# Kernel optimization log

Measured on AMD Instinct MI355X. Metric: run time of the kernel, lower is better.

Reference implementation:

```python
import jax, jax.numpy as jnp
import numpy as np

NEG_INF = -1e9
LEAKY_SLOPE = 0.2


def setup_inputs() -> dict:
    key = jax.random.key(0)
    k1, k2, k3, k4, k5 = jax.random.split(key, 5)
    B, N, F_in, F_out = 8, 2048, 256, 256
    x = jax.random.normal(k1, (B, N, F_in), dtype=jnp.float32)
    adj = jax.random.randint(k2, (B, N, N), 0, 2, dtype=jnp.int32)
    W = jax.random.normal(k3, (F_out, F_in), dtype=jnp.float32) * 0.05
    a_src = jax.random.normal(k4, (F_out,), dtype=jnp.float32) * 0.05
    a_dst = jax.random.normal(k5, (F_out,), dtype=jnp.float32) * 0.05
    return {"x": x, "adj": adj, "W": W, "a_src": a_src, "a_dst": a_dst}


def reference(x, adj, W, a_src, a_dst):
    # h: (B, N, F_out)
    h = jnp.einsum("bnf,of->bno", x, W)
    # a([h_i ; h_j]) == h_i @ a_src + h_j @ a_dst  (avoids O(N^2, 2F) concat)
    s_src = h @ a_src  # (B, N) score contribution of row node i
    s_dst = h @ a_dst  # (B, N) score contribution of col node j
    e = s_src[:, :, None] + s_dst[:, None, :]  # (B, N, N)
    e = jax.nn.leaky_relu(e, negative_slope=LEAKY_SLOPE)
    e = jnp.where(adj == 0, jnp.float32(NEG_INF), e)
    alpha = jax.nn.softmax(e, axis=-1)  # dropout is identity in eval mode
    h_prime = jnp.einsum("bij,bjo->bio", alpha, h)
    return h_prime
```

## Files before the change

### kernel.cpp

```cpp
#include <hip/hip_runtime.h>
#include <hip/hip_bf16.h>
#include <cstdint>
#include <cstddef>

typedef __attribute__((ext_vector_type(8))) short short8;
typedef __attribute__((ext_vector_type(4))) short short4v;
typedef __attribute__((ext_vector_type(4))) float floatx4;

#define LOG2E 1.44269504088896340736f

__device__ __forceinline__ unsigned short f2bf(float f) {
    unsigned u = __float_as_uint(f);
    u += 0x7FFFu + ((u >> 16) & 1u);
    return (unsigned short)(u >> 16);
}
__device__ __forceinline__ float bf2f(unsigned short s) {
    return __uint_as_float(((unsigned)s) << 16);
}

__global__ __launch_bounds__(256) void wprep(const float* __restrict__ W,
                                             unsigned short* __restrict__ Wb) {
    int t = blockIdx.x * 256 + threadIdx.x;
    float4 v = ((const float4*)W)[t];
    short4v s;
    s[0] = (short)f2bf(v.x); s[1] = (short)f2bf(v.y);
    s[2] = (short)f2bf(v.z); s[3] = (short)f2bf(v.w);
    ((short4v*)Wb)[t] = s;
}

__global__ __launch_bounds__(256) void gemm_h(const float* __restrict__ x,
                                              const unsigned short* __restrict__ Wb,
                                              unsigned short* __restrict__ hT) {
    const int w = threadIdx.x >> 6, lane = threadIdx.x & 63;
    const int q = lane >> 4, t16 = lane & 15;
    const int jrow = blockIdx.x * 64 + w * 16 + t16;
    const int ob   = blockIdx.y * 64;

    floatx4 acc[4] = {};
#pragma unroll
    for (int kb = 0; kb < 8; ++kb) {
        const int k0 = kb * 32 + q * 8;
        const float4* ax = (const float4*)(x + (size_t)jrow * 256 + k0);
        float4 a0 = ax[0], a1 = ax[1];
        short8 af;
        af[0] = (short)f2bf(a0.x); af[1] = (short)f2bf(a0.y);
        af[2] = (short)f2bf(a0.z); af[3] = (short)f2bf(a0.w);
        af[4] = (short)f2bf(a1.x); af[5] = (short)f2bf(a1.y);
        af[6] = (short)f2bf(a1.z); af[7] = (short)f2bf(a1.w);
#pragma unroll
        for (int ct = 0; ct < 4; ++ct) {
            short8 bf = *(const short8*)(Wb + (size_t)(ob + ct * 16 + t16) * 256 + k0);
            acc[ct] = __builtin_amdgcn_mfma_f32_16x16x32_bf16(af, bf, acc[ct], 0, 0, 0);
        }
    }
    const int jbase = blockIdx.x * 64 + w * 16 + q * 4;
    const int b = jbase >> 11, jj = jbase & 2047;
#pragma unroll
    for (int ct = 0; ct < 4; ++ct) {
        const int o = ob + ct * 16 + t16;
        short4v sv;
        sv[0] = (short)f2bf(acc[ct][0]);
        sv[1] = (short)f2bf(acc[ct][1]);
        sv[2] = (short)f2bf(acc[ct][2]);
        sv[3] = (short)f2bf(acc[ct][3]);
        *(short4v*)(hT + ((size_t)b * 256 + o) * 2048 + jj) = sv;
    }
}

__global__ __launch_bounds__(512) void s_kernel(const unsigned short* __restrict__ hT,
                                                const float* __restrict__ a_src,
                                                const float* __restrict__ a_dst,
                                                float* __restrict__ s_src,
                                                float* __restrict__ s_dst) {
    const int jl = threadIdx.x & 63;
    const int og = threadIdx.x >> 6;
    const int jg = blockIdx.x * 64 + jl;
    const int b = jg >> 11, jj = jg & 2047;
    const unsigned short* base = hT + (size_t)b * 256 * 2048 + jj;
    float ps = 0.f, pd = 0.f;
#pragma unroll 8
    for (int u = 0; u < 32; ++u) {
        const int o = og * 32 + u;
        float h = bf2f(base[(size_t)o * 2048]);
        ps = __fmaf_rn(h, a_src[o], ps);
        pd = __fmaf_rn(h, a_dst[o], pd);
    }
    __shared__ float rs[512], rd[512];
    rs[threadIdx.x] = ps; rd[threadIdx.x] = pd;
    __syncthreads();
    if (threadIdx.x < 64) {
        float a = 0.f, d = 0.f;
#pragma unroll
        for (int g = 0; g < 8; ++g) { a += rs[g * 64 + jl]; d += rd[g * 64 + jl]; }
        s_src[jg] = a; s_dst[jg] = d;
    }
}

__global__ __launch_bounds__(256, 2) void attn(const unsigned short* __restrict__ hT,
                                               const int* __restrict__ adj,
                                               const float* __restrict__ s_src,
                                               const float* __restrict__ s_dst,
                                               float* __restrict__ out) {
    const int tid = threadIdx.x;
    const int w = tid >> 6, lane = tid & 63;
    const int q = lane >> 4, t16 = lane & 15;
    const int b = blockIdx.y;
    const int i0 = blockIdx.x * 32;

    __shared__ float sd_lds[2048];
    __shared__ float si_lds[32];
    __shared__ unsigned short p_lds[2][32][136];
    __shared__ float lred[32][33];
    __shared__ float rl_lds[32];

    const float* sdb = s_dst + (size_t)b * 2048;
#pragma unroll
    for (int k = 0; k < 2; ++k) {
        int idx = (k * 256 + tid) * 4;
        float4 v = *(const float4*)(sdb + idx);
        v.x *= LOG2E; v.y *= LOG2E; v.z *= LOG2E; v.w *= LOG2E;
        *(float4*)(&sd_lds[idx]) = v;
    }
    if (tid < 32) si_lds[tid] = s_src[(size_t)b * 2048 + i0 + tid] * LOG2E;
    __syncthreads();

    const int rg = tid >> 5;
    const int jc = (tid & 31) * 4;
    const int* adjb = adj + ((size_t)b * 2048 + i0) * 2048;
    float si[4];
#pragma unroll
    for (int k = 0; k < 4; ++k) si[k] = si_lds[rg + 8 * k];

    float lsum[4] = {0.f, 0.f, 0.f, 0.f};
    int4 adjv[4];

    const unsigned short* hTw = hT + ((size_t)b * 256 + w * 64 + t16) * 2048 + q * 8;
    floatx4 accO[2][4] = {};

#pragma unroll
    for (int k = 0; k < 4; ++k)
        adjv[k] = *(const int4*)(adjb + (size_t)(rg + 8 * k) * 2048 + jc);
    {
        float4 sdv = *(const float4*)(&sd_lds[jc]);
        float sdl[4] = {sdv.x, sdv.y, sdv.z, sdv.w};
        unsigned short* pb = &p_lds[0][0][0];
#pragma unroll
        for (int k = 0; k < 4; ++k) {
            int mv[4] = {adjv[k].x, adjv[k].y, adjv[k].z, adjv[k].w};
            short4v sv;
#pragma unroll
            for (int e = 0; e < 4; ++e) {
                float t = si[k] + sdl[e];
                float lr = fmaxf(t, 0.2f * t);
                float pe = __builtin_amdgcn_exp2f(lr);
                pe = (mv[e] != 0) ? pe : 0.0f;
                unsigned short pu = f2bf(pe);
                sv[e] = (short)pu;
                lsum[k] += bf2f(pu);
            }
            *(short4v*)(pb + (rg + 8 * k) * 136 + jc) = sv;
        }
    }
    __syncthreads();

    for (int c = 0; c < 16; ++c) {
        if (c < 15) {
#pragma unroll
            for (int k = 0; k < 4; ++k)
                adjv[k] = *(const int4*)(adjb + (size_t)(rg + 8 * k) * 2048 + (c + 1) * 128 + jc);
        }
        const unsigned short* pb = &p_lds[c & 1][0][0];
#pragma unroll
        for (int ks = 0; ks < 4; ++ks) {
            short8 bf0 = *(const short8*)(pb + t16 * 136 + ks * 32 + q * 8);
            short8 bf1 = *(const short8*)(pb + (16 + t16) * 136 + ks * 32 + q * 8);
#pragma unroll
            for (int ct = 0; ct < 4; ++ct) {
                short8 af = *(const short8*)(hTw + (size_t)ct * 16 * 2048 + c * 128 + ks * 32);
                accO[0][ct] = __builtin_amdgcn_mfma_f32_16x16x32_bf16(af, bf0, accO[0][ct], 0, 0, 0);
                accO[1][ct] = __builtin_amdgcn_mfma_f32_16x16x32_bf16(af, bf1, accO[1][ct], 0, 0, 0);
            }
        }
        if (c < 15) {
            float4 sdv = *(const float4*)(&sd_lds[(c + 1) * 128 + jc]);
            float sdl[4] = {sdv.x, sdv.y, sdv.z, sdv.w};
            unsigned short* pw = &p_lds[(c + 1) & 1][0][0];
#pragma unroll
            for (int k = 0; k < 4; ++k) {
                int mv[4] = {adjv[k].x, adjv[k].y, adjv[k].z, adjv[k].w};
                short4v sv;
#pragma unroll
                for (int e = 0; e < 4; ++e) {
                    float t = si[k] + sdl[e];
                    float lr = fmaxf(t, 0.2f * t);
                    float pe = __builtin_amdgcn_exp2f(lr);
                    pe = (mv[e] != 0) ? pe : 0.0f;
                    unsigned short pu = f2bf(pe);
                    sv[e] = (short)pu;
                    lsum[k] += bf2f(pu);
                }
                *(short4v*)(pw + (rg + 8 * k) * 136 + jc) = sv;
            }
        }
        __syncthreads();
    }

#pragma unroll
    for (int k = 0; k < 4; ++k) lred[rg + 8 * k][tid & 31] = lsum[k];
    __syncthreads();
    if (tid < 32) {
        float s = 0.f;
#pragma unroll
        for (int u = 0; u < 32; ++u) s += lred[tid][u];
        rl_lds[tid] = (s > 0.f) ? 1.0f / s : 0.0f;
    }
    __syncthreads();

#pragma unroll
    for (int it = 0; it < 2; ++it) {
        const float rl = rl_lds[it * 16 + t16];
        float* orow = out + ((size_t)b * 2048 + i0 + it * 16 + t16) * 256 + w * 64 + q * 4;
#pragma unroll
        for (int ct = 0; ct < 4; ++ct) {
            floatx4 v = accO[it][ct] * rl;
            *(floatx4*)(orow + ct * 16) = v;
        }
    }
}

extern "C" void kernel_launch(void* const* d_in, const int* in_sizes, int n_in,
                              void* d_out, int out_size, void* d_ws, size_t ws_size,
                              hipStream_t stream) {
    const float* x     = (const float*)d_in[0];
    const int*   adj   = (const int*)d_in[1];
    const float* W     = (const float*)d_in[2];
    const float* a_src = (const float*)d_in[3];
    const float* a_dst = (const float*)d_in[4];
    float* out = (float*)d_out;

    unsigned short* hT = (unsigned short*)d_ws;
    float* s_src = (float*)((char*)d_ws + (size_t)8 * 1024 * 1024);
    float* s_dst = s_src + 16384;
    unsigned short* Wb = (unsigned short*)(s_dst + 16384);

    wprep<<<64, 256, 0, stream>>>(W, Wb);
    gemm_h<<<dim3(256, 4), 256, 0, stream>>>(x, Wb, hT);
    s_kernel<<<256, 512, 0, stream>>>(hT, a_src, a_dst, s_src, s_dst);
    attn<<<dim3(64, 8), 256, 0, stream>>>(hT, adj, s_src, s_dst, out);
}
```

Baseline: 291.2 us.

## Fuse score projection into GEMM and retile attention with LDS-staged h and 64-row tiles

The projection GEMM now computes all 256 output features per block, staging bf16 W through LDS. It computes s_src/s_dst in its epilogue with shuffle reductions, which removes the separate s_kernel launch and its strided re-read of hT. The attention kernel switches to 64 query rows per block with 32-column chunks, staging h tiles in double-buffered LDS instead of reading them straight from global memory. The intent is to cut redundant global traffic and a launch. The cost is larger per-block register and LDS use, plus a barrier on every one of 64 chunks instead of 16.

```diff
diff --git a/kernel.cpp b/kernel.cpp
--- a/kernel.cpp
+++ b/kernel.cpp
@@ -6,6 +6,7 @@
 typedef __attribute__((ext_vector_type(8))) short short8;
 typedef __attribute__((ext_vector_type(4))) short short4v;
 typedef __attribute__((ext_vector_type(4))) float floatx4;
+typedef unsigned short ushort_t;
 
 #define LOG2E 1.44269504088896340736f
 
@@ -19,7 +20,7 @@
 }
 
 __global__ __launch_bounds__(256) void wprep(const float* __restrict__ W,
-                                             unsigned short* __restrict__ Wb) {
+                                             ushort_t* __restrict__ Wb) {
     int t = blockIdx.x * 256 + threadIdx.x;
     float4 v = ((const float4*)W)[t];
     short4v s;
@@ -29,35 +30,60 @@
 }
 
 __global__ __launch_bounds__(256) void gemm_h(const float* __restrict__ x,
-                                              const unsigned short* __restrict__ Wb,
-                                              unsigned short* __restrict__ hT) {
-    const int w = threadIdx.x >> 6, lane = threadIdx.x & 63;
+                                              const ushort_t* __restrict__ Wb,
+                                              ushort_t* __restrict__ hT,
+                                              const float* __restrict__ a_src,
+                                              const float* __restrict__ a_dst,
+                                              float* __restrict__ s_src,
+                                              float* __restrict__ s_dst) {
+    const int tid = threadIdx.x;
+    const int w = tid >> 6, lane = tid & 63;
     const int q = lane >> 4, t16 = lane & 15;
+
+    __shared__ ushort_t wt[256][72];
+
     const int jrow = blockIdx.x * 64 + w * 16 + t16;
-    const int ob   = blockIdx.y * 64;
-
-    floatx4 acc[4] = {};
+    const float* xr = x + (size_t)jrow * 256 + q * 8;
+    short8 af[8];
 #pragma unroll
     for (int kb = 0; kb < 8; ++kb) {
-        const int k0 = kb * 32 + q * 8;
-        const float4* ax = (const float4*)(x + (size_t)jrow * 256 + k0);
-        float4 a0 = ax[0], a1 = ax[1];
-        short8 af;
-        af[0] = (short)f2bf(a0.x); af[1] = (short)f2bf(a0.y);
-        af[2] = (short)f2bf(a0.z); af[3] = (short)f2bf(a0.w);
-        af[4] = (short)f2bf(a1.x); af[5] = (short)f2bf(a1.y);
-        af[6] = (short)f2bf(a1.z); af[7] = (short)f2bf(a1.w);
-#pragma unroll
-        for (int ct = 0; ct < 4; ++ct) {
-            short8 bf = *(const short8*)(Wb + (size_t)(ob + ct * 16 + t16) * 256 + k0);
-            acc[ct] = __builtin_amdgcn_mfma_f32_16x16x32_bf16(af, bf, acc[ct], 0, 0, 0);
-        }
-    }
+        float4 v0 = *(const float4*)(xr + kb * 32);
+        float4 v1 = *(const float4*)(xr + kb * 32 + 4);
+        short8 a;
+        a[0] = (short)f2bf(v0.x); a[1] = (short)f2bf(v0.y);
+        a[2] = (short)f2bf(v0.z); a[3] = (short)f2bf(v0.w);
+        a[4] = (short)f2bf(v1.x); a[5] = (short)f2bf(v1.y);
+        a[6] = (short)f2bf(v1.z); a[7] = (short)f2bf(v1.w);
+        af[kb] = a;
+    }
+
+    floatx4 acc[16] = {};
+#pragma unroll
+    for (int kp = 0; kp < 4; ++kp) {
+        if (kp) __syncthreads();
+#pragma unroll
+        for (int r = 0; r < 8; ++r) {
+            int G = tid + 256 * r;
+            int row = G >> 3, g = G & 7;
+            int4 wv = *(const int4*)(Wb + (size_t)row * 256 + kp * 64 + g * 8);
+            *(int4*)(&wt[row][g * 8]) = wv;
+        }
+        __syncthreads();
+#pragma unroll
+        for (int ks = 0; ks < 2; ++ks) {
+#pragma unroll
+            for (int ct = 0; ct < 16; ++ct) {
+                short8 bf = *(const short8*)(&wt[ct * 16 + t16][ks * 32 + q * 8]);
+                acc[ct] = __builtin_amdgcn_mfma_f32_16x16x32_bf16(af[kp * 2 + ks], bf, acc[ct], 0, 0, 0);
+            }
+        }
+    }
+
     const int jbase = blockIdx.x * 64 + w * 16 + q * 4;
     const int b = jbase >> 11, jj = jbase & 2047;
 #pragma unroll
-    for (int ct = 0; ct < 4; ++ct) {
-        const int o = ob + ct * 16 + t16;
+    for (int ct = 0; ct < 16; ++ct) {
+        const int o = ct * 16 + t16;
         short4v sv;
         sv[0] = (short)f2bf(acc[ct][0]);
         sv[1] = (short)f2bf(acc[ct][1]);
@@ -65,53 +91,51 @@
         sv[3] = (short)f2bf(acc[ct][3]);
         *(short4v*)(hT + ((size_t)b * 256 + o) * 2048 + jj) = sv;
     }
-}
-
-__global__ __launch_bounds__(512) void s_kernel(const unsigned short* __restrict__ hT,
-                                                const float* __restrict__ a_src,
-                                                const float* __restrict__ a_dst,
-                                                float* __restrict__ s_src,
-                                                float* __restrict__ s_dst) {
-    const int jl = threadIdx.x & 63;
-    const int og = threadIdx.x >> 6;
-    const int jg = blockIdx.x * 64 + jl;
-    const int b = jg >> 11, jj = jg & 2047;
-    const unsigned short* base = hT + (size_t)b * 256 * 2048 + jj;
-    float ps = 0.f, pd = 0.f;
-#pragma unroll 8
-    for (int u = 0; u < 32; ++u) {
-        const int o = og * 32 + u;
-        float h = bf2f(base[(size_t)o * 2048]);
-        ps = __fmaf_rn(h, a_src[o], ps);
-        pd = __fmaf_rn(h, a_dst[o], pd);
-    }
-    __shared__ float rs[512], rd[512];
-    rs[threadIdx.x] = ps; rd[threadIdx.x] = pd;
-    __syncthreads();
-    if (threadIdx.x < 64) {
-        float a = 0.f, d = 0.f;
-#pragma unroll
-        for (int g = 0; g < 8; ++g) { a += rs[g * 64 + jl]; d += rd[g * 64 + jl]; }
-        s_src[jg] = a; s_dst[jg] = d;
-    }
-}
-
-__global__ __launch_bounds__(256, 2) void attn(const unsigned short* __restrict__ hT,
-                                               const int* __restrict__ adj,
-                                               const float* __restrict__ s_src,
-                                               const float* __restrict__ s_dst,
-                                               float* __restrict__ out) {
+
+    float psv[4] = {}, pdv[4] = {};
+#pragma unroll
+    for (int ct = 0; ct < 16; ++ct) {
+        const int o = ct * 16 + t16;
+        float as = a_src[o], ad = a_dst[o];
+#pragma unroll
+        for (int r = 0; r < 4; ++r) {
+            psv[r] = __fmaf_rn(acc[ct][r], as, psv[r]);
+            pdv[r] = __fmaf_rn(acc[ct][r], ad, pdv[r]);
+        }
+    }
+#pragma unroll
+    for (int m = 1; m < 16; m <<= 1) {
+#pragma unroll
+        for (int r = 0; r < 4; ++r) {
+            psv[r] += __shfl_xor(psv[r], m);
+            pdv[r] += __shfl_xor(pdv[r], m);
+        }
+    }
+    if (t16 == 0) {
+#pragma unroll
+        for (int r = 0; r < 4; ++r) {
+            s_src[jbase + r] = psv[r];
+            s_dst[jbase + r] = pdv[r];
+        }
+    }
+}
+
+__global__ __launch_bounds__(256) void attn(const ushort_t* __restrict__ hT,
+                                            const int* __restrict__ adj,
+                                            const float* __restrict__ s_src,
+                                            const float* __restrict__ s_dst,
+                                            float* __restrict__ out) {
     const int tid = threadIdx.x;
     const int w = tid >> 6, lane = tid & 63;
     const int q = lane >> 4, t16 = lane & 15;
-    const int b = blockIdx.y;
-    const int i0 = blockIdx.x * 32;
-
-    __shared__ float sd_lds[2048];
-    __shared__ float si_lds[32];
-    __shared__ unsigned short p_lds[2][32][136];
-    __shared__ float lred[32][33];
-    __shared__ float rl_lds[32];
+    const int b = blockIdx.x;
+    const int i0 = blockIdx.y * 64;
+
+    __shared__ ushort_t hts[2][256][40];
+    __shared__ ushort_t ps[2][64][40];
+    __shared__ float sdl[2048];
+    __shared__ float lred[64][5];
+    __shared__ float rll[64];
 
     const float* sdb = s_dst + (size_t)b * 2048;
 #pragma unroll
@@ -119,110 +143,85 @@
         int idx = (k * 256 + tid) * 4;
         float4 v = *(const float4*)(sdb + idx);
         v.x *= LOG2E; v.y *= LOG2E; v.z *= LOG2E; v.w *= LOG2E;
-        *(float4*)(&sd_lds[idx]) = v;
-    }
-    if (tid < 32) si_lds[tid] = s_src[(size_t)b * 2048 + i0 + tid] * LOG2E;
+        *(float4*)(&sdl[idx]) = v;
+    }
+
+    const int prow = tid & 63, jh = tid >> 6;
+    const float si = s_src[(size_t)b * 2048 + i0 + prow] * LOG2E;
+    const int* adjr = adj + ((size_t)b * 2048 + i0 + prow) * 2048 + jh * 8;
+    const ushort_t* hTg = hT + ((size_t)b * 256 + tid) * 2048;
+
+    const int osub = (w & 1) * 128, ih = (w >> 1) * 32;
+
+    floatx4 acc[8][2] = {};
+    float lsum = 0.f;
+    int4 hreg[4];
+    int4 a0, a1;
+
+#pragma unroll
+    for (int g = 0; g < 4; ++g)
+        hreg[g] = *(const int4*)(hTg + g * 8);
+    a0 = *(const int4*)(adjr);
+    a1 = *(const int4*)(adjr + 4);
     __syncthreads();
 
-    const int rg = tid >> 5;
-    const int jc = (tid & 31) * 4;
-    const int* adjb = adj + ((size_t)b * 2048 + i0) * 2048;
-    float si[4];
-#pragma unroll
-    for (int k = 0; k < 4; ++k) si[k] = si_lds[rg + 8 * k];
-
-    float lsum[4] = {0.f, 0.f, 0.f, 0.f};
-    int4 adjv[4];
-
-    const unsigned short* hTw = hT + ((size_t)b * 256 + w * 64 + t16) * 2048 + q * 8;
-    floatx4 accO[2][4] = {};
-
-#pragma unroll
-    for (int k = 0; k < 4; ++k)
-        adjv[k] = *(const int4*)(adjb + (size_t)(rg + 8 * k) * 2048 + jc);
-    {
-        float4 sdv = *(const float4*)(&sd_lds[jc]);
-        float sdl[4] = {sdv.x, sdv.y, sdv.z, sdv.w};
-        unsigned short* pb = &p_lds[0][0][0];
-#pragma unroll
-        for (int k = 0; k < 4; ++k) {
-            int mv[4] = {adjv[k].x, adjv[k].y, adjv[k].z, adjv[k].w};
-            short4v sv;
-#pragma unroll
-            for (int e = 0; e < 4; ++e) {
-                float t = si[k] + sdl[e];
+    for (int c = 0; c < 64; ++c) {
+        const int buf = c & 1;
+#pragma unroll
+        for (int g = 0; g < 4; ++g)
+            *(int4*)(&hts[buf][tid][g * 8]) = hreg[g];
+        {
+            float4 s0 = *(const float4*)(&sdl[c * 32 + jh * 8]);
+            float4 s1 = *(const float4*)(&sdl[c * 32 + jh * 8 + 4]);
+            float sdv[8] = {s0.x, s0.y, s0.z, s0.w, s1.x, s1.y, s1.z, s1.w};
+            int mv[8] = {a0.x, a0.y, a0.z, a0.w, a1.x, a1.y, a1.z, a1.w};
+            short8 pv;
+#pragma unroll
+            for (int e = 0; e < 8; ++e) {
+                float t = si + sdv[e];
                 float lr = fmaxf(t, 0.2f * t);
                 float pe = __builtin_amdgcn_exp2f(lr);
                 pe = (mv[e] != 0) ? pe : 0.0f;
-                unsigned short pu = f2bf(pe);
-                sv[e] = (short)pu;
-                lsum[k] += bf2f(pu);
+                unsigned short u = f2bf(pe);
+                lsum += bf2f(u);
+                pv[e] = (short)u;
             }
-            *(short4v*)(pb + (rg + 8 * k) * 136 + jc) = sv;
-        }
-    }
+            *(short8*)(&ps[buf][prow][jh * 8]) = pv;
+        }
+        if (c < 63) {
+#pragma unroll
+            for (int g = 0; g < 4; ++g)
+                hreg[g] = *(const int4*)(hTg + (c + 1) * 32 + g * 8);
+            a0 = *(const int4*)(adjr + (c + 1) * 32);
+            a1 = *(const int4*)(adjr + (c + 1) * 32 + 4);
+        }
+        __syncthreads();
+        short8 bf0 = *(const short8*)(&ps[buf][ih + t16][q * 8]);
+        short8 bf1 = *(const short8*)(&ps[buf][ih + 16 + t16][q * 8]);
+#pragma unroll
+        for (int ct = 0; ct < 8; ++ct) {
+            short8 af = *(const short8*)(&hts[buf][osub + ct * 16 + t16][q * 8]);
+            acc[ct][0] = __builtin_amdgcn_mfma_f32_16x16x32_bf16(af, bf0, acc[ct][0], 0, 0, 0);
+            acc[ct][1] = __builtin_amdgcn_mfma_f32_16x16x32_bf16(af, bf1, acc[ct][1], 0, 0, 0);
+        }
+    }
+
+    lred[prow][jh] = lsum;
     __syncthreads();
-
-    for (int c = 0; c < 16; ++c) {
-        if (c < 15) {
-#pragma unroll
-            for (int k = 0; k < 4; ++k)
-                adjv[k] = *(const int4*)(adjb + (size_t)(rg + 8 * k) * 2048 + (c + 1) * 128 + jc);
-        }
-        const unsigned short* pb = &p_lds[c & 1][0][0];
-#pragma unroll
-        for (int ks = 0; ks < 4; ++ks) {
-            short8 bf0 = *(const short8*)(pb + t16 * 136 + ks * 32 + q * 8);
-            short8 bf1 = *(const short8*)(pb + (16 + t16) * 136 + ks * 32 + q * 8);
-#pragma unroll
-            for (int ct = 0; ct < 4; ++ct) {
-                short8 af = *(const short8*)(hTw + (size_t)ct * 16 * 2048 + c * 128 + ks * 32);
-                accO[0][ct] = __builtin_amdgcn_mfma_f32_16x16x32_bf16(af, bf0, accO[0][ct], 0, 0, 0);
-                accO[1][ct] = __builtin_amdgcn_mfma_f32_16x16x32_bf16(af, bf1, accO[1][ct], 0, 0, 0);
-            }
-        }
-        if (c < 15) {
-            float4 sdv = *(const float4*)(&sd_lds[(c + 1) * 128 + jc]);
-            float sdl[4] = {sdv.x, sdv.y, sdv.z, sdv.w};
-            unsigned short* pw = &p_lds[(c + 1) & 1][0][0];
-#pragma unroll
-            for (int k = 0; k < 4; ++k) {
-                int mv[4] = {adjv[k].x, adjv[k].y, adjv[k].z, adjv[k].w};
-                short4v sv;
-#pragma unroll
-                for (int e = 0; e < 4; ++e) {
-                    float t = si[k] + sdl[e];
-                    float lr = fmaxf(t, 0.2f * t);
-                    float pe = __builtin_amdgcn_exp2f(lr);
-                    pe = (mv[e] != 0) ? pe : 0.0f;
-                    unsigned short pu = f2bf(pe);
-                    sv[e] = (short)pu;
-                    lsum[k] += bf2f(pu);
-                }
-                *(short4v*)(pw + (rg + 8 * k) * 136 + jc) = sv;
-            }
-        }
-        __syncthreads();
-    }
-
-#pragma unroll
-    for (int k = 0; k < 4; ++k) lred[rg + 8 * k][tid & 31] = lsum[k];
+    if (tid < 64) {
+        float s = lred[tid][0] + lred[tid][1] + lred[tid][2] + lred[tid][3];
+        rll[tid] = (s > 0.f) ? 1.0f / s : 0.0f;
+    }
     __syncthreads();
-    if (tid < 32) {
-        float s = 0.f;
-#pragma unroll
-        for (int u = 0; u < 32; ++u) s += lred[tid][u];
-        rl_lds[tid] = (s > 0.f) ? 1.0f / s : 0.0f;
-    }
-    __syncthreads();
 
 #pragma unroll
     for (int it = 0; it < 2; ++it) {
-        const float rl = rl_lds[it * 16 + t16];
-        float* orow = out + ((size_t)b * 2048 + i0 + it * 16 + t16) * 256 + w * 64 + q * 4;
-#pragma unroll
-        for (int ct = 0; ct < 4; ++ct) {
-            floatx4 v = accO[it][ct] * rl;
+        const int i = ih + it * 16 + t16;
+        const float rl = rll[i];
+        float* orow = out + ((size_t)b * 2048 + i0 + i) * 256 + osub + q * 4;
+#pragma unroll
+        for (int ct = 0; ct < 8; ++ct) {
+            floatx4 v = acc[ct][it] * rl;
             *(floatx4*)(orow + ct * 16) = v;
         }
     }
@@ -238,13 +237,13 @@
     const float* a_dst = (const float*)d_in[4];
     float* out = (float*)d_out;
 
-    unsigned short* hT = (unsigned short*)d_ws;
-    float* s_src = (float*)((char*)d_ws + (size_t)8 * 1024 * 1024);
+    char* ws = (char*)d_ws;
+    ushort_t* hT = (ushort_t*)ws;
+    float* s_src = (float*)(ws + (size_t)8 * 1024 * 1024);
     float* s_dst = s_src + 16384;
-    unsigned short* Wb = (unsigned short*)(s_dst + 16384);
+    ushort_t* Wb = (ushort_t*)(s_dst + 16384);
 
     wprep<<<64, 256, 0, stream>>>(W, Wb);
-    gemm_h<<<dim3(256, 4), 256, 0, stream>>>(x, Wb, hT);
-    s_kernel<<<256, 512, 0, stream>>>(hT, a_src, a_dst, s_src, s_dst);
-    attn<<<dim3(64, 8), 256, 0, stream>>>(hT, adj, s_src, s_dst, out);
-}
+    gemm_h<<<256, 256, 0, stream>>>(x, Wb, hT, a_src, a_dst, s_src, s_dst);
+    attn<<<dim3(8, 32), 256, 0, stream>>>(hT, adj, s_src, s_dst, out);
+}
```

Result: faster. 274.4 us (-5.8%).
